# Kernel optimization log

Hardware: AMD Instinct MI355X
Metric: run time of the kernel (lower is better)

## Reference

```python
import jax, jax.numpy as jnp
import numpy as np

B, T, C, H = 2, 2048, 1024, 16
HD = C // H
EPS = 1e-5


def _gelu_tanh(x):
    # 0.5*x*(1+tanh(sqrt(2/pi)*(x+0.044715*x^3)))
    c = jnp.sqrt(jnp.asarray(2.0 / np.pi, dtype=x.dtype))
    return 0.5 * x * (1.0 + jnp.tanh(c * (x + 0.044715 * x * x * x)))


def _layernorm(x, g, b):
    mu = jnp.mean(x, axis=-1, keepdims=True)
    var = jnp.mean(jnp.square(x - mu), axis=-1, keepdims=True)
    return (x - mu) * jax.lax.rsqrt(var + EPS) * g + b


def setup_inputs() -> dict:
    key = jax.random.key(0)
    ks = jax.random.split(key, 8)
    s = lambda fan_in: 1.0 / np.sqrt(fan_in)
    return {
        "x": jax.random.normal(ks[0], (B, T, C), jnp.float32),
        "ln1_g": jnp.ones((C,), jnp.float32),
        "ln1_b": jnp.zeros((C,), jnp.float32),
        "W_attn": jax.random.normal(ks[1], (C, 3 * C), jnp.float32) * s(C),
        "b_attn": jnp.zeros((3 * C,), jnp.float32),
        "W_proj": jax.random.normal(ks[2], (C, C), jnp.float32) * s(C),
        "b_proj": jnp.zeros((C,), jnp.float32),
        "ln2_g": jnp.ones((C,), jnp.float32),
        "ln2_b": jnp.zeros((C,), jnp.float32),
        "W_fc": jax.random.normal(ks[3], (C, 4 * C), jnp.float32) * s(C),
        "b_fc": jnp.zeros((4 * C,), jnp.float32),
        "W_fc2": jax.random.normal(ks[4], (4 * C, C), jnp.float32) * s(4 * C),
        "b_fc2": jnp.zeros((C,), jnp.float32),
    }


def reference(x, ln1_g, ln1_b, W_attn, b_attn, W_proj, b_proj,
              ln2_g, ln2_b, W_fc, b_fc, W_fc2, b_fc2):
    # --- attention branch (pre-LN) ---
    h = _layernorm(x, ln1_g, ln1_b)
    qkv = h @ W_attn + b_attn                      # [B,T,3C]
    q, k, v = jnp.split(qkv, 3, axis=2)
    q = q.reshape(B, T, H, HD).transpose(0, 2, 1, 3)  # [B,H,T,HD]
    k = k.reshape(B, T, H, HD).transpose(0, 2, 1, 3)
    v = v.reshape(B, T, H, HD).transpose(0, 2, 1, 3)
    att = jnp.einsum('bhqd,bhkd->bhqk', q, k) / jnp.sqrt(jnp.asarray(HD, x.dtype))
    causal = jnp.tril(jnp.ones((T, T), bool))
    att = jnp.where(causal, att, jnp.asarray(-jnp.inf, att.dtype))
    att = jax.nn.softmax(att, axis=-1)
    y = jnp.einsum('bhqk,bhkd->bhqd', att, v)      # [B,H,T,HD]
    y = y.transpose(0, 2, 1, 3).reshape(B, T, C)
    x = x + (y @ W_proj + b_proj)
    # --- MLP branch (pre-LN) ---
    h = _layernorm(x, ln2_g, ln2_b)
    h = _gelu_tanh(h @ W_fc + b_fc)
    x = x + (h @ W_fc2 + b_fc2)
    return x
```

## Files before the change

### kernel.cpp

```cpp
#include <hip/hip_runtime.h>
#include <hip/hip_bf16.h>
#include <cstdint>
#include <cstddef>

#define B_  2
#define T_  2048
#define C_  1024
#define H_  16
#define HD_ 64
#define M_TOT 4096

typedef __bf16 bf16x8 __attribute__((ext_vector_type(8)));
typedef float  f32x4  __attribute__((ext_vector_type(4)));
typedef unsigned short u16;

__device__ __forceinline__ u16 f2bf(float f) {
  __hip_bfloat16 h = __float2bfloat16(f);
  return __builtin_bit_cast(u16, h);
}

__device__ __forceinline__ void async_cp16(const u16* g, u16* l) {
  __builtin_amdgcn_global_load_lds(
      (const __attribute__((address_space(1))) void*)g,
      (__attribute__((address_space(3))) void*)l, 16, 0, 0);
}

__device__ __forceinline__ float gelu_f(float x) {
  const float z = 0.7978845608028654f * (x + 0.044715f * x * x * x);
  return x / (1.0f + __expf(-2.0f * z));
}

__global__ __launch_bounds__(256) void ln_bf16_kernel(
    const float* __restrict__ x, const float* __restrict__ g,
    const float* __restrict__ b, u16* __restrict__ out) {
  const int row = blockIdx.x;
  const int tid = threadIdx.x;
  const float4 v = reinterpret_cast<const float4*>(x)[row * 256 + tid];
  float s  = v.x + v.y + v.z + v.w;
  float sq = v.x * v.x + v.y * v.y + v.z * v.z + v.w * v.w;
#pragma unroll
  for (int off = 32; off > 0; off >>= 1) {
    s  += __shfl_xor(s, off);
    sq += __shfl_xor(sq, off);
  }
  __shared__ float red[8];
  const int wave = tid >> 6;
  if ((tid & 63) == 0) { red[wave] = s; red[4 + wave] = sq; }
  __syncthreads();
  s  = red[0] + red[1] + red[2] + red[3];
  sq = red[4] + red[5] + red[6] + red[7];
  const float mu   = s * (1.0f / 1024.0f);
  const float rstd = rsqrtf(sq * (1.0f / 1024.0f) - mu * mu + 1e-5f);
  const float4 gv = reinterpret_cast<const float4*>(g)[tid];
  const float4 bv = reinterpret_cast<const float4*>(b)[tid];
  ushort4 o;
  o.x = f2bf((v.x - mu) * rstd * gv.x + bv.x);
  o.y = f2bf((v.y - mu) * rstd * gv.y + bv.y);
  o.z = f2bf((v.z - mu) * rstd * gv.z + bv.z);
  o.w = f2bf((v.w - mu) * rstd * gv.w + bv.w);
  reinterpret_cast<ushort4*>(out)[row * 256 + tid] = o;
}

__global__ __launch_bounds__(256) void transpose_bf16_kernel(
    const float* __restrict__ W, u16* __restrict__ Wt, int K, int N) {
  __shared__ float tile[32][33];
  const int n0 = blockIdx.x * 32, k0 = blockIdx.y * 32;
  const int tx = threadIdx.x & 31;
  const int ty = threadIdx.x >> 5;
#pragma unroll
  for (int i = 0; i < 4; ++i)
    tile[ty + 8 * i][tx] = W[(k0 + ty + 8 * i) * (size_t)N + n0 + tx];
  __syncthreads();
#pragma unroll
  for (int i = 0; i < 4; ++i)
    Wt[(n0 + ty + 8 * i) * (size_t)K + k0 + tx] = f2bf(tile[tx][ty + 8 * i]);
}

template <int MODE, int BM>
__global__ __launch_bounds__(256, 2) void gemm_kernel(
    const u16* __restrict__ A, const u16* __restrict__ Bt,
    const float* __restrict__ bias, const float* __restrict__ resid,
    float* __restrict__ outf, u16* __restrict__ outb,
    u16* __restrict__ qo, u16* __restrict__ ko, u16* __restrict__ vto,
    int M, int N, int K, int logPer) {
  constexpr int MT = BM / 32;
  constexpr int AI = BM / 32;
  __shared__ __align__(16) u16 As[BM * 64];
  __shared__ __align__(16) u16 Bs[128 * 64];
  const int tid  = threadIdx.x;
  const int wave = tid >> 6, lane = tid & 63;
  const int col  = lane & 15, quad = lane >> 4;
  const int wm   = wave >> 1, wn = wave & 1;

  const int flat = blockIdx.y * gridDim.x + blockIdx.x;
  const int xcd = flat & 7, sl = flat >> 3;
  const int per = 1 << logPer;
  const int bm = (xcd << logPer) + (sl & (per - 1));
  const int bn = sl >> logPer;

  const int srow = lane >> 3, sc8 = lane & 7;
  const int kcs = (sc8 ^ srow) * 8;
  const u16* ap = A  + (size_t)(bm * BM + wave * (BM / 4) + srow) * K + kcs;
  const u16* bp = Bt + (size_t)(bn * 128 + wave * 32 + srow) * K + kcs;
  u16* as_dst = As + wave * (BM / 4) * 64;
  u16* bs_dst = Bs + wave * 2048;

  f32x4 acc[MT][4] = {};

  for (int k0 = 0; k0 < K; k0 += 64) {
    __syncthreads();
#pragma unroll
    for (int i = 0; i < AI; ++i)
      async_cp16(ap + k0 + i * 8 * (size_t)K, as_dst + i * 512);
#pragma unroll
    for (int i = 0; i < 4; ++i)
      async_cp16(bp + k0 + i * 8 * (size_t)K, bs_dst + i * 512);
    __syncthreads();
#pragma unroll
    for (int kh = 0; kh < 2; ++kh) {
      const int ks = kh * 4;
      bf16x8 af[MT], bf[4];
#pragma unroll
      for (int mt = 0; mt < MT; ++mt) {
        const int row = wm * (BM / 2) + mt * 16 + col;
        af[mt] = *reinterpret_cast<const bf16x8*>(&As[row * 64 + ((ks + quad) ^ (col & 7)) * 8]);
      }
#pragma unroll
      for (int nt = 0; nt < 4; ++nt) {
        const int row = wn * 64 + nt * 16 + col;
        bf[nt] = *reinterpret_cast<const bf16x8*>(&Bs[row * 64 + ((ks + quad) ^ (col & 7)) * 8]);
      }
#pragma unroll
      for (int mt = 0; mt < MT; ++mt)
#pragma unroll
        for (int nt = 0; nt < 4; ++nt)
          acc[mt][nt] = __builtin_amdgcn_mfma_f32_16x16x32_bf16(af[mt], bf[nt], acc[mt][nt], 0, 0, 0);
    }
  }

#pragma unroll
  for (int mt = 0; mt < MT; ++mt) {
#pragma unroll
    for (int r = 0; r < 4; ++r) {
      const int grow = bm * BM + wm * (BM / 2) + mt * 16 + quad * 4 + r;
#pragma unroll
      for (int nt = 0; nt < 4; ++nt) {
        const int gcol = bn * 128 + wn * 64 + nt * 16 + col;
        const float val = acc[mt][nt][r] + bias[gcol];
        if constexpr (MODE == 0) {
          outb[(size_t)grow * N + gcol] = f2bf(gelu_f(val));
        } else if constexpr (MODE == 1) {
          outf[(size_t)grow * N + gcol] = resid[(size_t)grow * N + gcol] + val;
        } else {
          const int which = gcol >> 10, c = gcol & 1023;
          const int hh = c >> 6, dd = c & 63;
          const int bb = grow >> 11, tt = grow & 2047;
          if (which == 0)
            qo[((bb * H_ + hh) * (size_t)T_ + tt) * HD_ + dd] = f2bf(val * 0.125f);
          else if (which == 1)
            ko[((bb * H_ + hh) * (size_t)T_ + tt) * HD_ + dd] = f2bf(val);
          else
            vto[((bb * H_ + hh) * (size_t)HD_ + dd) * T_ + tt] = f2bf(val);
        }
      }
    }
  }
}

#define PSTR 68
__global__ __launch_bounds__(256, 4) void attn_kernel(
    const u16* __restrict__ q, const u16* __restrict__ k,
    const u16* __restrict__ vt, u16* __restrict__ y) {
  const int bh  = blockIdx.x;
  const int tid = threadIdx.x;
  const int wave = tid >> 6, lane = tid & 63;
  const int col = lane & 15, quad = lane >> 4;
  const int b = bh >> 4, h = bh & 15;

  __shared__ __align__(16) u16 Klds[64 * PSTR];
  __shared__ __align__(16) u16 Vtlds[64 * PSTR];
  __shared__ __align__(16) u16 Plds[4 * 16 * PSTR];

  bf16x8 ones;
#pragma unroll
  for (int jj = 0; jj < 8; ++jj) ones[jj] = (__bf16)1.0f;

  const int srow = tid >> 3, spart = tid & 7;
  u16* pw = Plds + wave * 16 * PSTR;
  const u16* kbase  = k  + (size_t)bh * T_ * HD_ + srow * HD_ + spart * 8;
  const u16* vtbase = vt + (size_t)bh * HD_ * T_ + srow * T_ + spart * 8;

  for (int t = 0; t < 2; ++t) {
    const int qt = (t == 0) ? (T_ / 64 - 1 - blockIdx.y) : blockIdx.y;
    const int r0w = qt * 64 + wave * 16;

    bf16x8 aq[2];
#pragma unroll
    for (int j = 0; j < 2; ++j)
      aq[j] = *reinterpret_cast<const bf16x8*>(
          &q[((size_t)bh * T_ + r0w + col) * HD_ + j * 32 + quad * 8]);

    f32x4 o[4] = {};
    f32x4 l_acc = {};
    const int kb_last = qt * 64;

    uint4 kv0, kv1, kv2, kv3;
    kv0 = *reinterpret_cast<const uint4*>(kbase);
    kv1 = *reinterpret_cast<const uint4*>(kbase + 32 * HD_);
    kv2 = *reinterpret_cast<const uint4*>(vtbase);
    kv3 = *reinterpret_cast<const uint4*>(vtbase + 32 * T_);

    for (int kb = 0; kb <= kb_last; kb += 64) {
      *reinterpret_cast<uint4*>(&Klds[srow * PSTR + spart * 8])        = kv0;
      *reinterpret_cast<uint4*>(&Klds[(srow + 32) * PSTR + spart * 8]) = kv1;
      *reinterpret_cast<uint4*>(&Vtlds[srow * PSTR + spart * 8])        = kv2;
      *reinterpret_cast<uint4*>(&Vtlds[(srow + 32) * PSTR + spart * 8]) = kv3;
      __syncthreads();

      if (kb < kb_last) {
        const int nk = kb + 64;
        kv0 = *reinterpret_cast<const uint4*>(kbase + (size_t)nk * HD_);
        kv1 = *reinterpret_cast<const uint4*>(kbase + (size_t)nk * HD_ + 32 * HD_);
        kv2 = *reinterpret_cast<const uint4*>(vtbase + nk);
        kv3 = *reinterpret_cast<const uint4*>(vtbase + 32 * T_ + nk);
      }

      f32x4 s[4];
#pragma unroll
      for (int n = 0; n < 4; ++n) {
        const bf16x8 bk0 = *reinterpret_cast<const bf16x8*>(&Klds[(n * 16 + col) * PSTR + quad * 8]);
        const bf16x8 bk1 = *reinterpret_cast<const bf16x8*>(&Klds[(n * 16 + col) * PSTR + 32 + quad * 8]);
        f32x4 z = {};
        z = __builtin_amdgcn_mfma_f32_16x16x32_bf16(aq[0], bk0, z, 0, 0, 0);
        s[n] = __builtin_amdgcn_mfma_f32_16x16x32_bf16(aq[1], bk1, z, 0, 0, 0);
      }

      const bool domask = (kb == kb_last);
#pragma unroll
      for (int n = 0; n < 4; ++n) {
#pragma unroll
        for (int r = 0; r < 4; ++r) {
          float sv = s[n][r];
          if (domask) {
            const int key = kb + n * 16 + col;
            const int row = r0w + quad * 4 + r;
            sv = (key <= row) ? sv : -1e30f;
          }
          pw[(quad * 4 + r) * PSTR + n * 16 + col] = f2bf(__expf(sv));
        }
      }
      __builtin_amdgcn_s_waitcnt(0xC07F);

      const bf16x8 ap0 = *reinterpret_cast<const bf16x8*>(&pw[col * PSTR + quad * 8]);
      const bf16x8 ap1 = *reinterpret_cast<const bf16x8*>(&pw[col * PSTR + 32 + quad * 8]);
      l_acc = __builtin_amdgcn_mfma_f32_16x16x32_bf16(ap0, ones, l_acc, 0, 0, 0);
      l_acc = __builtin_amdgcn_mfma_f32_16x16x32_bf16(ap1, ones, l_acc, 0, 0, 0);
#pragma unroll
      for (int n = 0; n < 4; ++n) {
        const bf16x8 bv0 = *reinterpret_cast<const bf16x8*>(&Vtlds[(n * 16 + col) * PSTR + quad * 8]);
        const bf16x8 bv1 = *reinterpret_cast<const bf16x8*>(&Vtlds[(n * 16 + col) * PSTR + 32 + quad * 8]);
        o[n] = __builtin_amdgcn_mfma_f32_16x16x32_bf16(ap0, bv0, o[n], 0, 0, 0);
        o[n] = __builtin_amdgcn_mfma_f32_16x16x32_bf16(ap1, bv1, o[n], 0, 0, 0);
      }
      __syncthreads();
    }

#pragma unroll
    for (int r = 0; r < 4; ++r) {
      const int qrow = r0w + quad * 4 + r;
      const float inv = 1.0f / l_acc[r];
#pragma unroll
      for (int n = 0; n < 4; ++n)
        y[((size_t)b * T_ + qrow) * C_ + h * HD_ + n * 16 + col] = f2bf(o[n][r] * inv);
    }
  }
}

extern "C" void kernel_launch(void* const* d_in, const int* in_sizes, int n_in,
                              void* d_out, int out_size, void* d_ws, size_t ws_size,
                              hipStream_t stream) {
  const float* x      = (const float*)d_in[0];
  const float* ln1_g  = (const float*)d_in[1];
  const float* ln1_b  = (const float*)d_in[2];
  const float* W_attn = (const float*)d_in[3];
  const float* b_attn = (const float*)d_in[4];
  const float* W_proj = (const float*)d_in[5];
  const float* b_proj = (const float*)d_in[6];
  const float* ln2_g  = (const float*)d_in[7];
  const float* ln2_b  = (const float*)d_in[8];
  const float* W_fc   = (const float*)d_in[9];
  const float* b_fc   = (const float*)d_in[10];
  const float* W_fc2  = (const float*)d_in[11];
  const float* b_fc2  = (const float*)d_in[12];
  float* out = (float*)d_out;

  char* p = (char*)d_ws;
  auto alloc = [&](size_t bytes) {
    char* r = p;
    p += (bytes + 255) & ~(size_t)255;
    return r;
  };
  u16*   h1      = (u16*)alloc((size_t)M_TOT * C_ * 2);
  u16*   wt_attn = (u16*)alloc((size_t)3 * C_ * C_ * 2);
  u16*   wt_proj = (u16*)alloc((size_t)C_ * C_ * 2);
  u16*   wt_fc   = (u16*)alloc((size_t)4 * C_ * C_ * 2);
  u16*   wt_fc2  = (u16*)alloc((size_t)C_ * 4 * C_ * 2);
  u16*   qbuf    = (u16*)alloc((size_t)M_TOT * C_ * 2);
  u16*   kbuf    = (u16*)alloc((size_t)M_TOT * C_ * 2);
  u16*   vtbuf   = (u16*)alloc((size_t)M_TOT * C_ * 2);
  u16*   ybuf    = (u16*)alloc((size_t)M_TOT * C_ * 2);
  float* x2      = (float*)alloc((size_t)M_TOT * C_ * 4);
  u16*   h2      = (u16*)alloc((size_t)M_TOT * C_ * 2);
  u16*   act     = (u16*)alloc((size_t)M_TOT * 4 * C_ * 2);

  transpose_bf16_kernel<<<dim3(96, 32),  256, 0, stream>>>(W_attn, wt_attn, 1024, 3072);
  transpose_bf16_kernel<<<dim3(32, 32),  256, 0, stream>>>(W_proj, wt_proj, 1024, 1024);
  transpose_bf16_kernel<<<dim3(128, 32), 256, 0, stream>>>(W_fc,   wt_fc,   1024, 4096);
  transpose_bf16_kernel<<<dim3(32, 128), 256, 0, stream>>>(W_fc2,  wt_fc2,  4096, 1024);

  ln_bf16_kernel<<<M_TOT, 256, 0, stream>>>(x, ln1_g, ln1_b, h1);

  gemm_kernel<3, 128><<<dim3(24, 32), 256, 0, stream>>>(h1, wt_attn, b_attn, nullptr,
                                                        nullptr, nullptr, qbuf, kbuf, vtbuf,
                                                        4096, 3072, 1024, 2);
  attn_kernel<<<dim3(32, 16), 256, 0, stream>>>(qbuf, kbuf, vtbuf, ybuf);

  gemm_kernel<1, 64><<<dim3(8, 64), 256, 0, stream>>>(ybuf, wt_proj, b_proj, x,
                                                      x2, nullptr, nullptr, nullptr, nullptr,
                                                      4096, 1024, 1024, 3);
  ln_bf16_kernel<<<M_TOT, 256, 0, stream>>>(x2, ln2_g, ln2_b, h2);

  gemm_kernel<0, 128><<<dim3(32, 32), 256, 0, stream>>>(h2, wt_fc, b_fc, nullptr,
                                                        nullptr, act, nullptr, nullptr, nullptr,
                                                        4096, 4096, 1024, 2);
  gemm_kernel<1, 64><<<dim3(8, 64), 256, 0, stream>>>(act, wt_fc2, b_fc2, x2,
                                                      out, nullptr, nullptr, nullptr, nullptr,
                                                      4096, 1024, 4096, 3);
}
```

Measured before the change: 358.8 us.

## Enlarge attention query tile to 128 rows with double-buffered K/V LDS

Each attention block now handles one 128-row query tile, with each wave owning 32 rows. Every K/V tile loaded into LDS is therefore reused by twice as many query rows. K and V^T are double-buffered in LDS, so one barrier per iteration replaces two and the next tile's store overlaps the current compute. The previous pairing of a late and an early 64-row tile per block is dropped, so per-block work now varies with the causal position. Waves whose rows all lie before a key tile skip it, and launch bounds drop to 3 blocks per SM to allow more registers.

```diff
diff --git a/kernel.cpp b/kernel.cpp
--- a/kernel.cpp
+++ b/kernel.cpp
@@ -168,110 +168,137 @@
 }
 
 #define PSTR 68
-__global__ __launch_bounds__(256, 4) void attn_kernel(
+__global__ __launch_bounds__(256, 3) void attn_kernel(
     const u16* __restrict__ q, const u16* __restrict__ k,
     const u16* __restrict__ vt, u16* __restrict__ y) {
   const int bh  = blockIdx.x;
+  const int qt  = (T_ / 128 - 1) - blockIdx.y;
   const int tid = threadIdx.x;
   const int wave = tid >> 6, lane = tid & 63;
   const int col = lane & 15, quad = lane >> 4;
   const int b = bh >> 4, h = bh & 15;
-
-  __shared__ __align__(16) u16 Klds[64 * PSTR];
-  __shared__ __align__(16) u16 Vtlds[64 * PSTR];
-  __shared__ __align__(16) u16 Plds[4 * 16 * PSTR];
+  const int r0w = qt * 128 + wave * 32;
+
+  __shared__ __align__(16) u16 Klds[2][64 * PSTR];
+  __shared__ __align__(16) u16 Vtlds[2][64 * PSTR];
+  __shared__ __align__(16) u16 Plds[4 * 32 * PSTR];
+  u16* pw = Plds + wave * 32 * PSTR;
+
+  bf16x8 aq[2][2];
+#pragma unroll
+  for (int i = 0; i < 2; ++i)
+#pragma unroll
+    for (int j = 0; j < 2; ++j)
+      aq[i][j] = *reinterpret_cast<const bf16x8*>(
+          &q[((size_t)bh * T_ + r0w + i * 16 + col) * HD_ + j * 32 + quad * 8]);
 
   bf16x8 ones;
 #pragma unroll
   for (int jj = 0; jj < 8; ++jj) ones[jj] = (__bf16)1.0f;
 
+  f32x4 o[2][4] = {};
+  f32x4 l_acc[2] = {};
+
   const int srow = tid >> 3, spart = tid & 7;
-  u16* pw = Plds + wave * 16 * PSTR;
   const u16* kbase  = k  + (size_t)bh * T_ * HD_ + srow * HD_ + spart * 8;
   const u16* vtbase = vt + (size_t)bh * HD_ * T_ + srow * T_ + spart * 8;
 
-  for (int t = 0; t < 2; ++t) {
-    const int qt = (t == 0) ? (T_ / 64 - 1 - blockIdx.y) : blockIdx.y;
-    const int r0w = qt * 64 + wave * 16;
-
-    bf16x8 aq[2];
-#pragma unroll
-    for (int j = 0; j < 2; ++j)
-      aq[j] = *reinterpret_cast<const bf16x8*>(
-          &q[((size_t)bh * T_ + r0w + col) * HD_ + j * 32 + quad * 8]);
-
-    f32x4 o[4] = {};
-    f32x4 l_acc = {};
-    const int kb_last = qt * 64;
-
-    uint4 kv0, kv1, kv2, kv3;
-    kv0 = *reinterpret_cast<const uint4*>(kbase);
-    kv1 = *reinterpret_cast<const uint4*>(kbase + 32 * HD_);
-    kv2 = *reinterpret_cast<const uint4*>(vtbase);
-    kv3 = *reinterpret_cast<const uint4*>(vtbase + 32 * T_);
-
-    for (int kb = 0; kb <= kb_last; kb += 64) {
-      *reinterpret_cast<uint4*>(&Klds[srow * PSTR + spart * 8])        = kv0;
-      *reinterpret_cast<uint4*>(&Klds[(srow + 32) * PSTR + spart * 8]) = kv1;
-      *reinterpret_cast<uint4*>(&Vtlds[srow * PSTR + spart * 8])        = kv2;
-      *reinterpret_cast<uint4*>(&Vtlds[(srow + 32) * PSTR + spart * 8]) = kv3;
-      __syncthreads();
-
-      if (kb < kb_last) {
-        const int nk = kb + 64;
-        kv0 = *reinterpret_cast<const uint4*>(kbase + (size_t)nk * HD_);
-        kv1 = *reinterpret_cast<const uint4*>(kbase + (size_t)nk * HD_ + 32 * HD_);
-        kv2 = *reinterpret_cast<const uint4*>(vtbase + nk);
-        kv3 = *reinterpret_cast<const uint4*>(vtbase + 32 * T_ + nk);
-      }
-
-      f32x4 s[4];
+  const int kb_last = qt * 128 + 64;
+
+  uint4 kv0 = *reinterpret_cast<const uint4*>(kbase);
+  uint4 kv1 = *reinterpret_cast<const uint4*>(kbase + 32 * HD_);
+  uint4 kv2 = *reinterpret_cast<const uint4*>(vtbase);
+  uint4 kv3 = *reinterpret_cast<const uint4*>(vtbase + 32 * T_);
+  *reinterpret_cast<uint4*>(&Klds[0][srow * PSTR + spart * 8])         = kv0;
+  *reinterpret_cast<uint4*>(&Klds[0][(srow + 32) * PSTR + spart * 8])  = kv1;
+  *reinterpret_cast<uint4*>(&Vtlds[0][srow * PSTR + spart * 8])        = kv2;
+  *reinterpret_cast<uint4*>(&Vtlds[0][(srow + 32) * PSTR + spart * 8]) = kv3;
+
+  int cur = 0;
+  for (int kb = 0; kb <= kb_last; kb += 64) {
+    __syncthreads();
+
+    const bool haveNext = (kb < kb_last);
+    if (haveNext) {
+      const int nk = kb + 64;
+      kv0 = *reinterpret_cast<const uint4*>(kbase + (size_t)nk * HD_);
+      kv1 = *reinterpret_cast<const uint4*>(kbase + (size_t)nk * HD_ + 32 * HD_);
+      kv2 = *reinterpret_cast<const uint4*>(vtbase + nk);
+      kv3 = *reinterpret_cast<const uint4*>(vtbase + 32 * T_ + nk);
+    }
+
+    if (kb <= r0w + 31) {
+      f32x4 s[2][4];
 #pragma unroll
       for (int n = 0; n < 4; ++n) {
-        const bf16x8 bk0 = *reinterpret_cast<const bf16x8*>(&Klds[(n * 16 + col) * PSTR + quad * 8]);
-        const bf16x8 bk1 = *reinterpret_cast<const bf16x8*>(&Klds[(n * 16 + col) * PSTR + 32 + quad * 8]);
-        f32x4 z = {};
-        z = __builtin_amdgcn_mfma_f32_16x16x32_bf16(aq[0], bk0, z, 0, 0, 0);
-        s[n] = __builtin_amdgcn_mfma_f32_16x16x32_bf16(aq[1], bk1, z, 0, 0, 0);
-      }
-
-      const bool domask = (kb == kb_last);
+        const bf16x8 bk0 = *reinterpret_cast<const bf16x8*>(&Klds[cur][(n * 16 + col) * PSTR + quad * 8]);
+        const bf16x8 bk1 = *reinterpret_cast<const bf16x8*>(&Klds[cur][(n * 16 + col) * PSTR + 32 + quad * 8]);
+#pragma unroll
+        for (int i = 0; i < 2; ++i) {
+          f32x4 z = {};
+          z = __builtin_amdgcn_mfma_f32_16x16x32_bf16(aq[i][0], bk0, z, 0, 0, 0);
+          s[i][n] = __builtin_amdgcn_mfma_f32_16x16x32_bf16(aq[i][1], bk1, z, 0, 0, 0);
+        }
+      }
+
+      const bool domask = (kb + 63 > r0w);
+#pragma unroll
+      for (int i = 0; i < 2; ++i) {
+#pragma unroll
+        for (int n = 0; n < 4; ++n) {
+#pragma unroll
+          for (int r = 0; r < 4; ++r) {
+            float sv = s[i][n][r];
+            if (domask) {
+              const int key = kb + n * 16 + col;
+              const int row = r0w + i * 16 + quad * 4 + r;
+              sv = (key <= row) ? sv : -1e30f;
+            }
+            pw[(i * 16 + quad * 4 + r) * PSTR + n * 16 + col] = f2bf(__expf(sv));
+          }
+        }
+      }
+      __builtin_amdgcn_s_waitcnt(0xC07F);
+
+      bf16x8 ap0[2], ap1[2];
+#pragma unroll
+      for (int i = 0; i < 2; ++i) {
+        ap0[i] = *reinterpret_cast<const bf16x8*>(&pw[(i * 16 + col) * PSTR + quad * 8]);
+        ap1[i] = *reinterpret_cast<const bf16x8*>(&pw[(i * 16 + col) * PSTR + 32 + quad * 8]);
+        l_acc[i] = __builtin_amdgcn_mfma_f32_16x16x32_bf16(ap0[i], ones, l_acc[i], 0, 0, 0);
+        l_acc[i] = __builtin_amdgcn_mfma_f32_16x16x32_bf16(ap1[i], ones, l_acc[i], 0, 0, 0);
+      }
 #pragma unroll
       for (int n = 0; n < 4; ++n) {
-#pragma unroll
-        for (int r = 0; r < 4; ++r) {
-          float sv = s[n][r];
-          if (domask) {
-            const int key = kb + n * 16 + col;
-            const int row = r0w + quad * 4 + r;
-            sv = (key <= row) ? sv : -1e30f;
-          }
-          pw[(quad * 4 + r) * PSTR + n * 16 + col] = f2bf(__expf(sv));
+        const bf16x8 bv0 = *reinterpret_cast<const bf16x8*>(&Vtlds[cur][(n * 16 + col) * PSTR + quad * 8]);
+        const bf16x8 bv1 = *reinterpret_cast<const bf16x8*>(&Vtlds[cur][(n * 16 + col) * PSTR + 32 + quad * 8]);
+#pragma unroll
+        for (int i = 0; i < 2; ++i) {
+          o[i][n] = __builtin_amdgcn_mfma_f32_16x16x32_bf16(ap0[i], bv0, o[i][n], 0, 0, 0);
+          o[i][n] = __builtin_amdgcn_mfma_f32_16x16x32_bf16(ap1[i], bv1, o[i][n], 0, 0, 0);
         }
       }
-      __builtin_amdgcn_s_waitcnt(0xC07F);
-
-      const bf16x8 ap0 = *reinterpret_cast<const bf16x8*>(&pw[col * PSTR + quad * 8]);
-      const bf16x8 ap1 = *reinterpret_cast<const bf16x8*>(&pw[col * PSTR + 32 + quad * 8]);
-      l_acc = __builtin_amdgcn_mfma_f32_16x16x32_bf16(ap0, ones, l_acc, 0, 0, 0);
-      l_acc = __builtin_amdgcn_mfma_f32_16x16x32_bf16(ap1, ones, l_acc, 0, 0, 0);
-#pragma unroll
-      for (int n = 0; n < 4; ++n) {
-        const bf16x8 bv0 = *reinterpret_cast<const bf16x8*>(&Vtlds[(n * 16 + col) * PSTR + quad * 8]);
-        const bf16x8 bv1 = *reinterpret_cast<const bf16x8*>(&Vtlds[(n * 16 + col) * PSTR + 32 + quad * 8]);
-        o[n] = __builtin_amdgcn_mfma_f32_16x16x32_bf16(ap0, bv0, o[n], 0, 0, 0);
-        o[n] = __builtin_amdgcn_mfma_f32_16x16x32_bf16(ap1, bv1, o[n], 0, 0, 0);
-      }
-      __syncthreads();
-    }
-
+    }
+
+    if (haveNext) {
+      const int nxt = cur ^ 1;
+      *reinterpret_cast<uint4*>(&Klds[nxt][srow * PSTR + spart * 8])         = kv0;
+      *reinterpret_cast<uint4*>(&Klds[nxt][(srow + 32) * PSTR + spart * 8])  = kv1;
+      *reinterpret_cast<uint4*>(&Vtlds[nxt][srow * PSTR + spart * 8])        = kv2;
+      *reinterpret_cast<uint4*>(&Vtlds[nxt][(srow + 32) * PSTR + spart * 8]) = kv3;
+    }
+    cur ^= 1;
+  }
+
+#pragma unroll
+  for (int i = 0; i < 2; ++i) {
 #pragma unroll
     for (int r = 0; r < 4; ++r) {
-      const int qrow = r0w + quad * 4 + r;
-      const float inv = 1.0f / l_acc[r];
+      const int qrow = r0w + i * 16 + quad * 4 + r;
+      const float inv = 1.0f / l_acc[i][r];
 #pragma unroll
       for (int n = 0; n < 4; ++n)
-        y[((size_t)b * T_ + qrow) * C_ + h * HD_ + n * 16 + col] = f2bf(o[n][r] * inv);
+        y[((size_t)b * T_ + qrow) * C_ + h * HD_ + n * 16 + col] = f2bf(o[i][n][r] * inv);
     }
   }
 }
```

Measured after the change: 365.6 us. About the same (+1.9%).

## Split attention into 32-row query tiles with 2-wave blocks, one tile per block

Applied to the files above, without the earlier changes.

The attention kernel previously ran 256-thread blocks that each handled a pair of 64-row query tiles (one late, one early) to balance causal work. It now launches 128-thread blocks that each handle a single 32-row query tile, ordered longest-first, giving 2048 blocks instead of 512. K/V staging is redone for 128 threads, and the causal mask check becomes per-wave. The goal is more parallelism and finer load balance across CUs, at the cost of loading each K/V tile into LDS more times and having fewer waves share each staged tile.

```diff
diff --git a/kernel.cpp b/kernel.cpp
--- a/kernel.cpp
+++ b/kernel.cpp
@@ -168,111 +168,112 @@
 }
 
 #define PSTR 68
-__global__ __launch_bounds__(256, 4) void attn_kernel(
+__global__ __launch_bounds__(128, 3) void attn_kernel(
     const u16* __restrict__ q, const u16* __restrict__ k,
     const u16* __restrict__ vt, u16* __restrict__ y) {
   const int bh  = blockIdx.x;
+  const int qt  = (T_ / 32 - 1) - blockIdx.y;
   const int tid = threadIdx.x;
   const int wave = tid >> 6, lane = tid & 63;
   const int col = lane & 15, quad = lane >> 4;
   const int b = bh >> 4, h = bh & 15;
+  const int r0w = qt * 32 + wave * 16;
 
   __shared__ __align__(16) u16 Klds[64 * PSTR];
   __shared__ __align__(16) u16 Vtlds[64 * PSTR];
-  __shared__ __align__(16) u16 Plds[4 * 16 * PSTR];
+  __shared__ __align__(16) u16 Plds[2 * 16 * PSTR];
+  u16* pw = Plds + wave * 16 * PSTR;
+
+  bf16x8 aq[2];
+#pragma unroll
+  for (int j = 0; j < 2; ++j)
+    aq[j] = *reinterpret_cast<const bf16x8*>(
+        &q[((size_t)bh * T_ + r0w + col) * HD_ + j * 32 + quad * 8]);
 
   bf16x8 ones;
 #pragma unroll
   for (int jj = 0; jj < 8; ++jj) ones[jj] = (__bf16)1.0f;
 
+  f32x4 o[4] = {};
+  f32x4 l_acc = {};
+
   const int srow = tid >> 3, spart = tid & 7;
-  u16* pw = Plds + wave * 16 * PSTR;
-  const u16* kbase  = k  + (size_t)bh * T_ * HD_ + srow * HD_ + spart * 8;
-  const u16* vtbase = vt + (size_t)bh * HD_ * T_ + srow * T_ + spart * 8;
-
-  for (int t = 0; t < 2; ++t) {
-    const int qt = (t == 0) ? (T_ / 64 - 1 - blockIdx.y) : blockIdx.y;
-    const int r0w = qt * 64 + wave * 16;
-
-    bf16x8 aq[2];
-#pragma unroll
-    for (int j = 0; j < 2; ++j)
-      aq[j] = *reinterpret_cast<const bf16x8*>(
-          &q[((size_t)bh * T_ + r0w + col) * HD_ + j * 32 + quad * 8]);
-
-    f32x4 o[4] = {};
-    f32x4 l_acc = {};
-    const int kb_last = qt * 64;
-
-    uint4 kv0, kv1, kv2, kv3;
-    kv0 = *reinterpret_cast<const uint4*>(kbase);
-    kv1 = *reinterpret_cast<const uint4*>(kbase + 32 * HD_);
-    kv2 = *reinterpret_cast<const uint4*>(vtbase);
-    kv3 = *reinterpret_cast<const uint4*>(vtbase + 32 * T_);
-
-    for (int kb = 0; kb <= kb_last; kb += 64) {
-      *reinterpret_cast<uint4*>(&Klds[srow * PSTR + spart * 8])        = kv0;
-      *reinterpret_cast<uint4*>(&Klds[(srow + 32) * PSTR + spart * 8]) = kv1;
-      *reinterpret_cast<uint4*>(&Vtlds[srow * PSTR + spart * 8])        = kv2;
-      *reinterpret_cast<uint4*>(&Vtlds[(srow + 32) * PSTR + spart * 8]) = kv3;
-      __syncthreads();
-
-      if (kb < kb_last) {
-        const int nk = kb + 64;
-        kv0 = *reinterpret_cast<const uint4*>(kbase + (size_t)nk * HD_);
-        kv1 = *reinterpret_cast<const uint4*>(kbase + (size_t)nk * HD_ + 32 * HD_);
-        kv2 = *reinterpret_cast<const uint4*>(vtbase + nk);
-        kv3 = *reinterpret_cast<const uint4*>(vtbase + 32 * T_ + nk);
-      }
-
-      f32x4 s[4];
-#pragma unroll
-      for (int n = 0; n < 4; ++n) {
-        const bf16x8 bk0 = *reinterpret_cast<const bf16x8*>(&Klds[(n * 16 + col) * PSTR + quad * 8]);
-        const bf16x8 bk1 = *reinterpret_cast<const bf16x8*>(&Klds[(n * 16 + col) * PSTR + 32 + quad * 8]);
-        f32x4 z = {};
-        z = __builtin_amdgcn_mfma_f32_16x16x32_bf16(aq[0], bk0, z, 0, 0, 0);
-        s[n] = __builtin_amdgcn_mfma_f32_16x16x32_bf16(aq[1], bk1, z, 0, 0, 0);
-      }
-
-      const bool domask = (kb == kb_last);
-#pragma unroll
-      for (int n = 0; n < 4; ++n) {
-#pragma unroll
-        for (int r = 0; r < 4; ++r) {
-          float sv = s[n][r];
-          if (domask) {
-            const int key = kb + n * 16 + col;
-            const int row = r0w + quad * 4 + r;
-            sv = (key <= row) ? sv : -1e30f;
-          }
-          pw[(quad * 4 + r) * PSTR + n * 16 + col] = f2bf(__expf(sv));
+  const u16* kbase  = k  + (size_t)bh * T_ * HD_ + (size_t)srow * HD_ + spart * 8;
+  const u16* vtbase = vt + (size_t)bh * HD_ * T_ + (size_t)srow * T_ + spart * 8;
+
+  const int kb_last = (qt >> 1) * 64;
+
+  uint4 kv[4], vv[4];
+#pragma unroll
+  for (int i = 0; i < 4; ++i) {
+    kv[i] = *reinterpret_cast<const uint4*>(kbase  + (size_t)(16 * i) * HD_);
+    vv[i] = *reinterpret_cast<const uint4*>(vtbase + (size_t)(16 * i) * T_);
+  }
+
+  for (int kb = 0; kb <= kb_last; kb += 64) {
+#pragma unroll
+    for (int i = 0; i < 4; ++i) {
+      *reinterpret_cast<uint4*>(&Klds[(srow + 16 * i) * PSTR + spart * 8])  = kv[i];
+      *reinterpret_cast<uint4*>(&Vtlds[(srow + 16 * i) * PSTR + spart * 8]) = vv[i];
+    }
+    __syncthreads();
+
+    if (kb < kb_last) {
+      const int nk = kb + 64;
+#pragma unroll
+      for (int i = 0; i < 4; ++i) {
+        kv[i] = *reinterpret_cast<const uint4*>(kbase  + (size_t)(nk + 16 * i) * HD_);
+        vv[i] = *reinterpret_cast<const uint4*>(vtbase + (size_t)(16 * i) * T_ + nk);
+      }
+    }
+
+    f32x4 s[4];
+#pragma unroll
+    for (int n = 0; n < 4; ++n) {
+      const bf16x8 bk0 = *reinterpret_cast<const bf16x8*>(&Klds[(n * 16 + col) * PSTR + quad * 8]);
+      const bf16x8 bk1 = *reinterpret_cast<const bf16x8*>(&Klds[(n * 16 + col) * PSTR + 32 + quad * 8]);
+      f32x4 z = {};
+      z = __builtin_amdgcn_mfma_f32_16x16x32_bf16(aq[0], bk0, z, 0, 0, 0);
+      s[n] = __builtin_amdgcn_mfma_f32_16x16x32_bf16(aq[1], bk1, z, 0, 0, 0);
+    }
+
+    const bool domask = (kb + 63 > r0w);
+#pragma unroll
+    for (int n = 0; n < 4; ++n) {
+#pragma unroll
+      for (int r = 0; r < 4; ++r) {
+        float sv = s[n][r];
+        if (domask) {
+          const int key = kb + n * 16 + col;
+          const int row = r0w + quad * 4 + r;
+          sv = (key <= row) ? sv : -1e30f;
         }
-      }
-      __builtin_amdgcn_s_waitcnt(0xC07F);
-
-      const bf16x8 ap0 = *reinterpret_cast<const bf16x8*>(&pw[col * PSTR + quad * 8]);
-      const bf16x8 ap1 = *reinterpret_cast<const bf16x8*>(&pw[col * PSTR + 32 + quad * 8]);
-      l_acc = __builtin_amdgcn_mfma_f32_16x16x32_bf16(ap0, ones, l_acc, 0, 0, 0);
-      l_acc = __builtin_amdgcn_mfma_f32_16x16x32_bf16(ap1, ones, l_acc, 0, 0, 0);
-#pragma unroll
-      for (int n = 0; n < 4; ++n) {
-        const bf16x8 bv0 = *reinterpret_cast<const bf16x8*>(&Vtlds[(n * 16 + col) * PSTR + quad * 8]);
-        const bf16x8 bv1 = *reinterpret_cast<const bf16x8*>(&Vtlds[(n * 16 + col) * PSTR + 32 + quad * 8]);
-        o[n] = __builtin_amdgcn_mfma_f32_16x16x32_bf16(ap0, bv0, o[n], 0, 0, 0);
-        o[n] = __builtin_amdgcn_mfma_f32_16x16x32_bf16(ap1, bv1, o[n], 0, 0, 0);
-      }
-      __syncthreads();
-    }
-
-#pragma unroll
-    for (int r = 0; r < 4; ++r) {
-      const int qrow = r0w + quad * 4 + r;
-      const float inv = 1.0f / l_acc[r];
-#pragma unroll
-      for (int n = 0; n < 4; ++n)
-        y[((size_t)b * T_ + qrow) * C_ + h * HD_ + n * 16 + col] = f2bf(o[n][r] * inv);
-    }
+        pw[(quad * 4 + r) * PSTR + n * 16 + col] = f2bf(__expf(sv));
+      }
+    }
+    __builtin_amdgcn_s_waitcnt(0xC07F);
+
+    const bf16x8 ap0 = *reinterpret_cast<const bf16x8*>(&pw[col * PSTR + quad * 8]);
+    const bf16x8 ap1 = *reinterpret_cast<const bf16x8*>(&pw[col * PSTR + 32 + quad * 8]);
+    l_acc = __builtin_amdgcn_mfma_f32_16x16x32_bf16(ap0, ones, l_acc, 0, 0, 0);
+    l_acc = __builtin_amdgcn_mfma_f32_16x16x32_bf16(ap1, ones, l_acc, 0, 0, 0);
+#pragma unroll
+    for (int n = 0; n < 4; ++n) {
+      const bf16x8 bv0 = *reinterpret_cast<const bf16x8*>(&Vtlds[(n * 16 + col) * PSTR + quad * 8]);
+      const bf16x8 bv1 = *reinterpret_cast<const bf16x8*>(&Vtlds[(n * 16 + col) * PSTR + 32 + quad * 8]);
+      o[n] = __builtin_amdgcn_mfma_f32_16x16x32_bf16(ap0, bv0, o[n], 0, 0, 0);
+      o[n] = __builtin_amdgcn_mfma_f32_16x16x32_bf16(ap1, bv1, o[n], 0, 0, 0);
+    }
+    __syncthreads();
+  }
+
+#pragma unroll
+  for (int r = 0; r < 4; ++r) {
+    const int qrow = r0w + quad * 4 + r;
+    const float inv = 1.0f / l_acc[r];
+#pragma unroll
+    for (int n = 0; n < 4; ++n)
+      y[((size_t)b * T_ + qrow) * C_ + h * HD_ + n * 16 + col] = f2bf(o[n][r] * inv);
   }
 }
 
@@ -323,7 +324,7 @@
   gemm_kernel<3, 128><<<dim3(24, 32), 256, 0, stream>>>(h1, wt_attn, b_attn, nullptr,
                                                         nullptr, nullptr, qbuf, kbuf, vtbuf,
                                                         4096, 3072, 1024, 2);
-  attn_kernel<<<dim3(32, 16), 256, 0, stream>>>(qbuf, kbuf, vtbuf, ybuf);
+  attn_kernel<<<dim3(32, 64), 128, 0, stream>>>(qbuf, kbuf, vtbuf, ybuf);
 
   gemm_kernel<1, 64><<<dim3(8, 64), 256, 0, stream>>>(ybuf, wt_proj, b_proj, x,
                                                       x2, nullptr, nullptr, nullptr, nullptr,
```

Measured after the change: 467.0 us. 30.1% more time.
